# Optimization experiments

Measured on AMD Instinct MI355X. Metric: run time of the kernel, lower is better.

## Reference

```python
import jax, jax.numpy as jnp
import numpy as np

B, S, H = 4, 2048, 1024
NH, HD, G = 16, 64, 8          # heads, head_dim, groups
GD = HD // G                   # group_dim = 8
SCALE_MIN, SCALE_MAX = 0.9, 1.1


def setup_inputs() -> dict:
    key = jax.random.key(0)
    ks = jax.random.split(key, 9)
    std = 1.0 / np.sqrt(H)
    return {
        "hidden_states": jax.random.normal(ks[0], (B, S, H), jnp.float32),
        "Wq": jax.random.normal(ks[1], (H, H), jnp.float32) * std,
        "bq": jax.random.normal(ks[2], (H,), jnp.float32) * std,
        "Wk": jax.random.normal(ks[3], (H, H), jnp.float32) * std,
        "bk": jax.random.normal(ks[4], (H,), jnp.float32) * std,
        "Wv": jax.random.normal(ks[5], (H, H), jnp.float32) * std,
        "bv": jax.random.normal(ks[6], (H,), jnp.float32) * std,
        "Ws": jax.random.normal(ks[7], (H, NH * G), jnp.float32) * std,
        "bs": jax.random.normal(ks[8], (NH * G,), jnp.float32) * std,
    }


def _shape_heads(x):
    # [B,S,H] -> [B,h,S,D]
    return x.reshape(B, S, NH, HD).transpose(0, 2, 1, 3)


def reference(hidden_states, Wq, bq, Wk, bk, Wv, bv, Ws, bs):
    Q = _shape_heads(hidden_states @ Wq + bq)
    K = _shape_heads(hidden_states @ Wk + bk)
    V = _shape_heads(hidden_states @ Wv + bv)

    # per-(head, group) dynamic scale in [scale_min, scale_max]
    s_logits = hidden_states @ Ws + bs                     # [B,S,h*g]
    s = jax.nn.sigmoid(s_logits) * (SCALE_MAX - SCALE_MIN) + SCALE_MIN
    s = s.reshape(B, S, NH, G).transpose(0, 2, 1, 3)       # [B,h,S,g]
    s = jnp.repeat(s, GD, axis=-1)                          # [B,h,S,D]

    Q = Q * s  # apply_to == 'q'

    attn_scores = jnp.einsum('bhsd,bhtd->bhst', Q, K) / np.sqrt(HD).astype(np.float32)
    attn_probs = jax.nn.softmax(attn_scores, axis=-1)
    context = jnp.einsum('bhst,bhtd->bhsd', attn_probs, V)
    context = context.transpose(0, 2, 1, 3).reshape(B, S, NH * HD)
    return context
```

## Files before the change

kernel.cpp:

```cpp
#include <hip/hip_runtime.h>
#include <hip/hip_bf16.h>
#include <stdint.h>

typedef short bf16x8 __attribute__((ext_vector_type(8)));
typedef float f32x4 __attribute__((ext_vector_type(4)));
typedef unsigned short u16;
typedef unsigned short u16x4 __attribute__((ext_vector_type(4)));
typedef unsigned short u16x8 __attribute__((ext_vector_type(8)));
typedef unsigned int u32x4v __attribute__((ext_vector_type(4)));

#define LOG2E 1.44269504088896f

#define Bz 4
#define Sz 2048
#define Hz 1024
#define NHz 16
#define HDz 64

__device__ __forceinline__ u16 f2bf(float f) {
  uint32_t u = __builtin_bit_cast(uint32_t, f);
  u += 0x7fffu + ((u >> 16) & 1u);
  return (u16)(u >> 16);
}
__device__ __forceinline__ float bf2f(u16 h) {
  uint32_t u = ((uint32_t)h) << 16;
  return __builtin_bit_cast(float, u);
}

__device__ __forceinline__ void gll16(const void* g, void* l) {
  __builtin_amdgcn_global_load_lds((const __attribute__((address_space(1))) void*)g,
                                   (__attribute__((address_space(3))) void*)l,
                                   16, 0, 0);
}

__global__ void k_cvt_x(const float* __restrict__ X, u16* __restrict__ Xb) {
  int i = blockIdx.x * 256 + threadIdx.x;
  float4 v = ((const float4*)X)[i];
  u16x4 r;
  r[0] = f2bf(v.x); r[1] = f2bf(v.y); r[2] = f2bf(v.z); r[3] = f2bf(v.w);
  ((u16x4*)Xb)[i] = r;
}

__global__ void k_cvt_w(const float* __restrict__ Wq, const float* __restrict__ Wk,
                        const float* __restrict__ Wv, const float* __restrict__ Ws,
                        u16* __restrict__ Wt) {
  __shared__ float tile[64][65];
  int n0 = blockIdx.x * 64, k0 = blockIdx.y * 64;
  const float* src; int ld, c0;
  if (n0 < 1024)      { src = Wq; ld = 1024; c0 = n0; }
  else if (n0 < 2048) { src = Wk; ld = 1024; c0 = n0 - 1024; }
  else if (n0 < 3072) { src = Wv; ld = 1024; c0 = n0 - 2048; }
  else                { src = Ws; ld = 128;  c0 = n0 - 3072; }
  int t = threadIdx.x;
  #pragma unroll
  for (int i = 0; i < 16; ++i) {
    int idx = t + i * 256; int r = idx >> 6, c = idx & 63;
    tile[r][c] = src[(size_t)(k0 + r) * ld + c0 + c];
  }
  __syncthreads();
  #pragma unroll
  for (int i = 0; i < 16; ++i) {
    int idx = t + i * 256; int rn = idx >> 6, ck = idx & 63;
    Wt[(size_t)(n0 + rn) * 1024 + k0 + ck] = f2bf(tile[ck][rn]);
  }
}

__launch_bounds__(512, 6)
__global__ void k_gemm(const u16* __restrict__ Xb, const u16* __restrict__ Wt,
                       const float* __restrict__ bq, const float* __restrict__ bk,
                       const float* __restrict__ bv, const float* __restrict__ bs,
                       u16* __restrict__ Qw, u16* __restrict__ Kw, u16* __restrict__ Vw,
                       float* __restrict__ Sw) {
  __shared__ u16 As[128 * 64];
  __shared__ u16 Bs[128 * 64];
  int t = threadIdx.x, lane = t & 63;
  int l15 = lane & 15, g = lane >> 4;
  int wave = t >> 6, wr = wave >> 2, wc = wave & 3;

  int p = blockIdx.x;
  int xcd = p & 7;
  int idx = p >> 3;
  int n_t = idx >> 3;
  int m_t = xcd * 8 + (idx & 7);
  int m0 = m_t * 128, n0 = n_t * 128;

  f32x4 acc[4][2];
  #pragma unroll
  for (int i = 0; i < 4; ++i)
    #pragma unroll
    for (int j = 0; j < 2; ++j) { f32x4 z = {0.f,0.f,0.f,0.f}; acc[i][j] = z; }

  int srow = t >> 3;
  int sob  = (t & 7) << 4;

  const char* Ag = (const char*)Xb;
  const char* Bg = (const char*)Wt;

  {
    int row = srow;
    int sb = sob ^ ((row & 7) << 4);
    gll16(Ag + (size_t)(m0 + row) * 2048 + sb, (char*)As + row * 128 + sob);
    gll16(Bg + (size_t)(n0 + row) * 2048 + sb, (char*)Bs + row * 128 + sob);
    row = 64 + srow;
    sb = sob ^ ((row & 7) << 4);
    gll16(Ag + (size_t)(m0 + row) * 2048 + sb, (char*)As + row * 128 + sob);
    gll16(Bg + (size_t)(n0 + row) * 2048 + sb, (char*)Bs + row * 128 + sob);
  }
  __syncthreads();

  for (int kt = 0; kt < 16; ++kt) {
    #pragma unroll
    for (int ksub = 0; ksub < 2; ++ksub) {
      bf16x8 af[4], bfr[2];
      #pragma unroll
      for (int ai = 0; ai < 4; ++ai) {
        int row = wr * 64 + ai * 16 + l15;
        af[ai] = *(const bf16x8*)((const char*)As + row * 128 +
                                  ((ksub * 64 + 16 * g) ^ ((row & 7) << 4)));
      }
      #pragma unroll
      for (int bj = 0; bj < 2; ++bj) {
        int row = wc * 32 + bj * 16 + l15;
        bfr[bj] = *(const bf16x8*)((const char*)Bs + row * 128 +
                                   ((ksub * 64 + 16 * g) ^ ((row & 7) << 4)));
      }
      #pragma unroll
      for (int ai = 0; ai < 4; ++ai)
        #pragma unroll
        for (int bj = 0; bj < 2; ++bj)
          acc[ai][bj] = __builtin_amdgcn_mfma_f32_16x16x32_bf16(af[ai], bfr[bj], acc[ai][bj], 0, 0, 0);
    }
    if (kt + 1 < 16) {
      __syncthreads();
      size_t kb = (size_t)(kt + 1) * 128;
      int row = srow;
      int sb = sob ^ ((row & 7) << 4);
      gll16(Ag + (size_t)(m0 + row) * 2048 + kb + sb, (char*)As + row * 128 + sob);
      gll16(Bg + (size_t)(n0 + row) * 2048 + kb + sb, (char*)Bs + row * 128 + sob);
      row = 64 + srow;
      sb = sob ^ ((row & 7) << 4);
      gll16(Ag + (size_t)(m0 + row) * 2048 + kb + sb, (char*)As + row * 128 + sob);
      gll16(Bg + (size_t)(n0 + row) * 2048 + kb + sb, (char*)Bs + row * 128 + sob);
      __syncthreads();
    }
  }

  #pragma unroll
  for (int ai = 0; ai < 4; ++ai) {
    #pragma unroll
    for (int bj = 0; bj < 2; ++bj) {
      #pragma unroll
      for (int r = 0; r < 4; ++r) {
        int m = m0 + wr * 64 + ai * 16 + ((lane >> 4) << 2) + r;
        int j = n0 + wc * 32 + bj * 16 + l15;
        float v = acc[ai][bj][r];
        int b = m >> 11, si = m & 2047;
        if (j < 3072) {
          float bias = (j < 1024) ? bq[j] : (j < 2048) ? bk[j - 1024] : bv[j - 2048];
          v += bias;
          int jj = j & 1023, h = jj >> 6, d = jj & 63;
          size_t dst = (((size_t)(b * NHz + h) * Sz + si) << 6) + d;
          u16 hv = f2bf(v);
          if (j < 1024) Qw[dst] = hv;
          else if (j < 2048) Kw[dst] = hv;
          else Vw[dst] = hv;
        } else {
          int c = j - 3072;
          v += bs[c];
          float sig = 1.0f / (1.0f + __expf(-v));
          Sw[(size_t)m * 128 + c] = (0.9f + 0.2f * sig) * 0.125f * LOG2E;
        }
      }
    }
  }
}

__global__ void k_scale_q(u16* __restrict__ Qw, const float* __restrict__ Sw) {
  int tid = blockIdx.x * 256 + threadIdx.x;
  size_t base = (size_t)tid * 8;
  int bh = (int)(base >> 17);
  int si = (int)((base >> 6) & 2047);
  int d0 = (int)(base & 63);
  int b = bh >> 4, h = bh & 15;
  float s = Sw[((size_t)(b * Sz + si)) * 128 + h * 8 + (d0 >> 3)];
  u16x8 v = *(u16x8*)(Qw + base);
  #pragma unroll
  for (int j = 0; j < 8; ++j) v[j] = f2bf(bf2f(v[j]) * s);
  *(u16x8*)(Qw + base) = v;
}

__global__ void k_trans_v(const u16* __restrict__ Vw, u16* __restrict__ Vt) {
  __shared__ u16 tile[64][65];
  int bh = blockIdx.y, s0 = blockIdx.x * 64;
  int t = threadIdx.x;
  const u16* src = Vw + ((size_t)bh * Sz + s0) * 64;
  #pragma unroll
  for (int i = 0; i < 16; ++i) {
    int idx = t + i * 256; int r = idx >> 6, c = idx & 63;
    tile[r][c] = src[r * 64 + c];
  }
  __syncthreads();
  u16* dst = Vt + (size_t)bh * 64 * Sz;
  #pragma unroll
  for (int i = 0; i < 16; ++i) {
    int idx = t + i * 256; int d = idx >> 6, ss = idx & 63;
    dst[(size_t)d * Sz + s0 + ss] = tile[ss][d];
  }
}

__launch_bounds__(256)
__global__ void k_attn(const u16* __restrict__ Qw, const u16* __restrict__ Kw,
                       const u16* __restrict__ Vt, const float* __restrict__ Swp,
                       float* __restrict__ out) {
  __shared__ u16 Kl[2][64 * 64];
  __shared__ u16 Vl[2][64 * 64];

  int t = threadIdx.x, lane = t & 63, wave = t >> 6;
  int l15 = lane & 15, g = lane >> 4;
  int bh = blockIdx.x, b = bh >> 4, h = bh & 15;
  int q0 = blockIdx.y * 256 + wave * 64;

  const u16* Qb = Qw + (size_t)bh * Sz * 64;
  const char* Kg = (const char*)(Kw + (size_t)bh * Sz * 64);
  const char* Vg = (const char*)(Vt + (size_t)bh * 64 * Sz);

  int pi15 = (l15 & 3) | ((l15 & 4) << 1) | ((l15 & 8) >> 1);

  int srow = t >> 3;
  int sobyte = (t & 7) << 4;

  bf16x8 qf[4][2];
  #pragma unroll
  for (int qi = 0; qi < 4; ++qi)
    #pragma unroll
    for (int ks = 0; ks < 2; ++ks)
      qf[qi][ks] = *(const bf16x8*)(Qb + (size_t)(q0 + 16 * qi + l15) * 64 + 32 * ks + 8 * g);
  if (Swp) {
    #pragma unroll
    for (int qi = 0; qi < 4; ++qi) {
      size_t m = (size_t)(b * Sz + q0 + 16 * qi + l15);
      #pragma unroll
      for (int ks = 0; ks < 2; ++ks) {
        float s = Swp[m * 128 + h * 8 + 4 * ks + g];
        bf16x8 q = qf[qi][ks];
        #pragma unroll
        for (int j = 0; j < 8; ++j) q[j] = (short)f2bf(bf2f((u16)q[j]) * s);
        qf[qi][ks] = q;
      }
    }
  }

  bf16x8 ones;
  #pragma unroll
  for (int j = 0; j < 8; ++j) ones[j] = (short)0x3F80;

  f32x4 o[4][4], lacc[4];
  #pragma unroll
  for (int qi = 0; qi < 4; ++qi) {
    f32x4 z = {0.f,0.f,0.f,0.f};
    lacc[qi] = z;
    #pragma unroll
    for (int nt = 0; nt < 4; ++nt) o[qi][nt] = z;
  }

  #pragma unroll
  for (int c = 0; c < 2; ++c) {
    int row = c * 32 + srow;
    int sw2 = (row & 7) << 4;
    gll16(Kg + (size_t)row * 128 + (sobyte ^ sw2), (char*)Kl[0] + row * 128 + sobyte);
    gll16(Vg + (size_t)row * (Sz * 2) + (sobyte ^ sw2), (char*)Vl[0] + row * 128 + sobyte);
  }
  __syncthreads();

  int cur = 0;
  for (int kv0 = 0; kv0 < Sz; kv0 += 64) {
    if (kv0 + 64 < Sz) {
      int nxt = cur ^ 1, kvn = kv0 + 64;
      #pragma unroll
      for (int c = 0; c < 2; ++c) {
        int row = c * 32 + srow;
        int sw2 = (row & 7) << 4;
        gll16(Kg + (size_t)(kvn + row) * 128 + (sobyte ^ sw2),
              (char*)Kl[nxt] + row * 128 + sobyte);
        gll16(Vg + (size_t)row * (Sz * 2) + (size_t)kvn * 2 + (sobyte ^ sw2),
              (char*)Vl[nxt] + row * 128 + sobyte);
      }
    }
    const char* Kb = (const char*)Kl[cur];
    const char* Vb = (const char*)Vl[cur];

    bf16x8 pa[4][2];
    #pragma unroll
    for (int qp = 0; qp < 2; ++qp) {
      f32x4 sc[2][4];
      __builtin_amdgcn_s_setprio(1);
      #pragma unroll
      for (int nt = 0; nt < 4; ++nt) {
        int row = 16 * nt + pi15;
        int sw2 = (row & 7) << 4;
        bf16x8 kf0 = *(const bf16x8*)(Kb + row * 128 + ((16 * g) ^ sw2));
        bf16x8 kf1 = *(const bf16x8*)(Kb + row * 128 + ((64 + 16 * g) ^ sw2));
        #pragma unroll
        for (int j = 0; j < 2; ++j) {
          f32x4 a = {0.f,0.f,0.f,0.f};
          a = __builtin_amdgcn_mfma_f32_16x16x32_bf16(kf0, qf[2 * qp + j][0], a, 0, 0, 0);
          a = __builtin_amdgcn_mfma_f32_16x16x32_bf16(kf1, qf[2 * qp + j][1], a, 0, 0, 0);
          sc[j][nt] = a;
        }
      }
      __builtin_amdgcn_s_setprio(0);
      #pragma unroll
      for (int j = 0; j < 2; ++j) {
        unsigned W0[4], W1[4];
        #pragma unroll
        for (int nt = 0; nt < 4; ++nt) {
          float p0 = __builtin_amdgcn_exp2f(sc[j][nt][0]);
          float p1 = __builtin_amdgcn_exp2f(sc[j][nt][1]);
          float p2 = __builtin_amdgcn_exp2f(sc[j][nt][2]);
          float p3 = __builtin_amdgcn_exp2f(sc[j][nt][3]);
          asm("v_cvt_pk_bf16_f32 %0, %1, %2" : "=v"(W0[nt]) : "v"(p0), "v"(p1));
          asm("v_cvt_pk_bf16_f32 %0, %1, %2" : "=v"(W1[nt]) : "v"(p2), "v"(p3));
        }
        #pragma unroll
        for (int ks = 0; ks < 2; ++ks) {
          unsigned x0 = W0[2 * ks], y0 = W0[2 * ks + 1];
          unsigned x1 = W1[2 * ks], y1 = W1[2 * ks + 1];
          asm("v_permlane32_swap_b32 %0, %1" : "+v"(x0), "+v"(y0));
          asm("v_permlane32_swap_b32 %0, %1" : "+v"(x1), "+v"(y1));
          u32x4v wv; wv[0] = x0; wv[1] = x1; wv[2] = y0; wv[3] = y1;
          pa[2 * qp + j][ks] = __builtin_bit_cast(bf16x8, wv);
        }
      }
    }

    __builtin_amdgcn_s_setprio(1);
    #pragma unroll
    for (int ks = 0; ks < 2; ++ks) {
      #pragma unroll
      for (int qi = 0; qi < 4; ++qi)
        lacc[qi] = __builtin_amdgcn_mfma_f32_16x16x32_bf16(pa[qi][ks], ones, lacc[qi], 0, 0, 0);
      #pragma unroll
      for (int nt = 0; nt < 4; ++nt) {
        int row = 16 * nt + l15;
        int sw2 = (row & 7) << 4;
        bf16x8 vf = *(const bf16x8*)(Vb + row * 128 + ((64 * ks + 16 * g) ^ sw2));
        #pragma unroll
        for (int qi = 0; qi < 4; ++qi)
          o[qi][nt] = __builtin_amdgcn_mfma_f32_16x16x32_bf16(pa[qi][ks], vf, o[qi][nt], 0, 0, 0);
      }
    }
    __builtin_amdgcn_s_setprio(0);
    __syncthreads();
    cur ^= 1;
  }

  #pragma unroll
  for (int qi = 0; qi < 4; ++qi) {
    #pragma unroll
    for (int r = 0; r < 4; ++r) {
      float inv = 1.0f / lacc[qi][r];
      #pragma unroll
      for (int nt = 0; nt < 4; ++nt)
        out[((size_t)(b * Sz + q0 + 16 * qi + 4 * g + r)) * (NHz * HDz) +
            h * 64 + 16 * nt + l15] = o[qi][nt][r] * inv;
    }
  }
}

extern "C" void kernel_launch(void* const* d_in, const int* in_sizes, int n_in,
                              void* d_out, int out_size, void* d_ws, size_t ws_size,
                              hipStream_t stream) {
  const float* X  = (const float*)d_in[0];
  const float* Wq = (const float*)d_in[1];
  const float* bq = (const float*)d_in[2];
  const float* Wk = (const float*)d_in[3];
  const float* bk = (const float*)d_in[4];
  const float* Wv = (const float*)d_in[5];
  const float* bv = (const float*)d_in[6];
  const float* Ws = (const float*)d_in[7];
  const float* bs = (const float*)d_in[8];
  float* out = (float*)d_out;

  char* ws = (char*)d_ws;
  u16* Qw = (u16*)(ws);
  u16* Kw = (u16*)(ws + (size_t)(16u << 20));
  u16* Vw = (u16*)(ws + (size_t)(32u << 20));
  u16* Vt = (u16*)(ws + (size_t)(48u << 20));

  char* ob = (char*)d_out;
  u16* Xb   = (u16*)ob;
  u16* Wt   = (u16*)(ob + (size_t)(16u << 20));

  bool fused = ws_size >= ((size_t)(64u << 20) + (size_t)(4u << 20));
  float* Sw = fused ? (float*)(ws + (size_t)(64u << 20))
                    : (float*)(ob + (size_t)(24u << 20));

  k_cvt_x<<<8192, 256, 0, stream>>>(X, Xb);
  k_cvt_w<<<dim3(50, 16), 256, 0, stream>>>(Wq, Wk, Wv, Ws, Wt);
  k_gemm<<<1600, 512, 0, stream>>>(Xb, Wt, bq, bk, bv, bs, Qw, Kw, Vw, Sw);
  if (!fused) k_scale_q<<<4096, 256, 0, stream>>>(Qw, Sw);
  k_trans_v<<<dim3(32, 64), 256, 0, stream>>>(Vw, Vt);
  k_attn<<<dim3(64, 8), 256, 0, stream>>>(Qw, Kw, Vt, fused ? Sw : nullptr, out);
}
```

Measured before the change: 180.0 us.

## Double-buffer LDS tiles in projection GEMM with split A/B prefetch

Converts the QKV/scale projection GEMM mainloop to double-buffered LDS. The next A tile is prefetched before the compute and the next B tile between the two k-substeps, using explicit vmcnt waits and a single barrier pair per iteration. This is meant to overlap global-to-LDS loads with MFMA work instead of stalling on a sync-load-sync sequence each iteration. It doubles LDS usage and lowers the occupancy hint from 6 to 4, and it adds s_setprio around the MFMA blocks.

```diff
diff --git a/kernel.cpp b/kernel.cpp
--- a/kernel.cpp
+++ b/kernel.cpp
@@ -65,14 +65,14 @@
   }
 }
 
-__launch_bounds__(512, 6)
+__launch_bounds__(512, 4)
 __global__ void k_gemm(const u16* __restrict__ Xb, const u16* __restrict__ Wt,
                        const float* __restrict__ bq, const float* __restrict__ bk,
                        const float* __restrict__ bv, const float* __restrict__ bs,
                        u16* __restrict__ Qw, u16* __restrict__ Kw, u16* __restrict__ Vw,
                        float* __restrict__ Sw) {
-  __shared__ u16 As[128 * 64];
-  __shared__ u16 Bs[128 * 64];
+  __shared__ u16 As[2][128 * 64];
+  __shared__ u16 Bs[2][128 * 64];
   int t = threadIdx.x, lane = t & 63;
   int l15 = lane & 15, g = lane >> 4;
   int wave = t >> 6, wr = wave >> 2, wc = wave & 3;
@@ -96,53 +96,90 @@
   const char* Ag = (const char*)Xb;
   const char* Bg = (const char*)Wt;
 
-  {
-    int row = srow;
-    int sb = sob ^ ((row & 7) << 4);
-    gll16(Ag + (size_t)(m0 + row) * 2048 + sb, (char*)As + row * 128 + sob);
-    gll16(Bg + (size_t)(n0 + row) * 2048 + sb, (char*)Bs + row * 128 + sob);
-    row = 64 + srow;
-    sb = sob ^ ((row & 7) << 4);
-    gll16(Ag + (size_t)(m0 + row) * 2048 + sb, (char*)As + row * 128 + sob);
-    gll16(Bg + (size_t)(n0 + row) * 2048 + sb, (char*)Bs + row * 128 + sob);
-  }
-  __syncthreads();
+  auto stageA = [&](int kt, int buf) {
+    size_t kb = (size_t)kt * 128;
+    #pragma unroll
+    for (int c = 0; c < 2; ++c) {
+      int row = c * 64 + srow;
+      int sb = sob ^ ((row & 7) << 4);
+      gll16(Ag + (size_t)(m0 + row) * 2048 + kb + sb, (char*)As[buf] + row * 128 + sob);
+    }
+  };
+  auto stageB = [&](int kt, int buf) {
+    size_t kb = (size_t)kt * 128;
+    #pragma unroll
+    for (int c = 0; c < 2; ++c) {
+      int row = c * 64 + srow;
+      int sb = sob ^ ((row & 7) << 4);
+      gll16(Bg + (size_t)(n0 + row) * 2048 + kb + sb, (char*)Bs[buf] + row * 128 + sob);
+    }
+  };
+
+  stageA(0, 0);
+  stageB(0, 0);
+  asm volatile("s_waitcnt vmcnt(0)" ::: "memory");
+  __builtin_amdgcn_s_barrier();
+  __builtin_amdgcn_sched_barrier(0);
 
   for (int kt = 0; kt < 16; ++kt) {
-    #pragma unroll
-    for (int ksub = 0; ksub < 2; ++ksub) {
+    int cur = kt & 1;
+    if (kt + 1 < 16) {
+      stageA(kt + 1, cur ^ 1);
+      asm volatile("s_waitcnt vmcnt(2)" ::: "memory");
+    } else if (kt > 0) {
+      asm volatile("s_waitcnt vmcnt(0)" ::: "memory");
+    }
+    __builtin_amdgcn_sched_barrier(0);
+    __builtin_amdgcn_s_barrier();
+    __builtin_amdgcn_sched_barrier(0);
+
+    const char* Ab = (const char*)As[cur];
+    const char* Bb = (const char*)Bs[cur];
+
+    {
       bf16x8 af[4], bfr[2];
       #pragma unroll
       for (int ai = 0; ai < 4; ++ai) {
         int row = wr * 64 + ai * 16 + l15;
-        af[ai] = *(const bf16x8*)((const char*)As + row * 128 +
-                                  ((ksub * 64 + 16 * g) ^ ((row & 7) << 4)));
+        af[ai] = *(const bf16x8*)(Ab + row * 128 + ((16 * g) ^ ((row & 7) << 4)));
       }
       #pragma unroll
       for (int bj = 0; bj < 2; ++bj) {
         int row = wc * 32 + bj * 16 + l15;
-        bfr[bj] = *(const bf16x8*)((const char*)Bs + row * 128 +
-                                   ((ksub * 64 + 16 * g) ^ ((row & 7) << 4)));
-      }
+        bfr[bj] = *(const bf16x8*)(Bb + row * 128 + ((16 * g) ^ ((row & 7) << 4)));
+      }
+      __builtin_amdgcn_s_setprio(1);
       #pragma unroll
       for (int ai = 0; ai < 4; ++ai)
         #pragma unroll
         for (int bj = 0; bj < 2; ++bj)
           acc[ai][bj] = __builtin_amdgcn_mfma_f32_16x16x32_bf16(af[ai], bfr[bj], acc[ai][bj], 0, 0, 0);
-    }
-    if (kt + 1 < 16) {
-      __syncthreads();
-      size_t kb = (size_t)(kt + 1) * 128;
-      int row = srow;
-      int sb = sob ^ ((row & 7) << 4);
-      gll16(Ag + (size_t)(m0 + row) * 2048 + kb + sb, (char*)As + row * 128 + sob);
-      gll16(Bg + (size_t)(n0 + row) * 2048 + kb + sb, (char*)Bs + row * 128 + sob);
-      row = 64 + srow;
-      sb = sob ^ ((row & 7) << 4);
-      gll16(Ag + (size_t)(m0 + row) * 2048 + kb + sb, (char*)As + row * 128 + sob);
-      gll16(Bg + (size_t)(n0 + row) * 2048 + kb + sb, (char*)Bs + row * 128 + sob);
-      __syncthreads();
-    }
+      __builtin_amdgcn_s_setprio(0);
+    }
+    if (kt + 1 < 16) stageB(kt + 1, cur ^ 1);
+    {
+      bf16x8 af[4], bfr[2];
+      #pragma unroll
+      for (int ai = 0; ai < 4; ++ai) {
+        int row = wr * 64 + ai * 16 + l15;
+        af[ai] = *(const bf16x8*)(Ab + row * 128 + ((64 + 16 * g) ^ ((row & 7) << 4)));
+      }
+      #pragma unroll
+      for (int bj = 0; bj < 2; ++bj) {
+        int row = wc * 32 + bj * 16 + l15;
+        bfr[bj] = *(const bf16x8*)(Bb + row * 128 + ((64 + 16 * g) ^ ((row & 7) << 4)));
+      }
+      __builtin_amdgcn_s_setprio(1);
+      #pragma unroll
+      for (int ai = 0; ai < 4; ++ai)
+        #pragma unroll
+        for (int bj = 0; bj < 2; ++bj)
+          acc[ai][bj] = __builtin_amdgcn_mfma_f32_16x16x32_bf16(af[ai], bfr[bj], acc[ai][bj], 0, 0, 0);
+      __builtin_amdgcn_s_setprio(0);
+    }
+    __builtin_amdgcn_sched_barrier(0);
+    __builtin_amdgcn_s_barrier();
+    __builtin_amdgcn_sched_barrier(0);
   }
 
   #pragma unroll
```

Measured after the change: 192.6 us. +7.0%, slower.
